# Kernel optimization log

Hardware: AMD Instinct MI355X
Metric: run time of the kernel (lower is better)

## Reference

```python
import jax, jax.numpy as jnp
import numpy as np
from jax import lax

# LIF parameters (norse defaults)
DT = 0.001
TAU_SYN_INV = 200.0
TAU_MEM_INV = 100.0
V_TH = 1.0
V_LEAK = 0.0
V_RESET = 0.0


def _spike(v_minus_th):
    # forward heaviside (surrogate grad only matters for bwd module)
    return (v_minus_th > 0).astype(v_minus_th.dtype)


def setup_inputs() -> dict:
    key = jax.random.key(0)
    ks = jax.random.split(key, 5)
    B, T, F, H, O = 256, 1000, 128, 256, 2
    x = jax.random.normal(ks[0], (B, T, F), dtype=jnp.float32)
    w_in = jax.random.normal(ks[1], (H, F), dtype=jnp.float32) / np.sqrt(F)
    w_rec = jax.random.normal(ks[2], (H, H), dtype=jnp.float32) / np.sqrt(H)
    fc_w = jax.random.normal(ks[3], (O, H), dtype=jnp.float32) / np.sqrt(H)
    fc_b = jnp.zeros((O,), dtype=jnp.float32)
    return {"x": x, "w_in": w_in, "w_rec": w_rec, "fc_w": fc_w, "fc_b": fc_b}


def reference(x, w_in, w_rec, fc_w, fc_b):
    B = x.shape[0]
    H = w_in.shape[0]
    # precompute feed-forward input currents for all timesteps: [B,T,H] -> [T,B,H]
    xw = jnp.einsum("btf,hf->bth", x, w_in)
    xw = jnp.swapaxes(xw, 0, 1)

    def step(carry, xt):
        v, i, z = carry
        # membrane decay toward leak + synaptic current integration
        v_dec = v + DT * TAU_MEM_INV * ((V_LEAK - v) + i)
        # synaptic current decay
        i_dec = i * (1.0 - DT * TAU_SYN_INV)
        # threshold / spike / reset
        z_new = _spike(v_dec - V_TH)
        v_new = (1.0 - z_new) * v_dec + z_new * V_RESET
        # inject feed-forward + recurrent current for next step
        i_new = i_dec + xt + z @ w_rec.T
        return (v_new, i_new, z_new), z_new

    zeros = jnp.zeros((B, H), dtype=x.dtype)
    _, zs = lax.scan(step, (zeros, zeros, zeros), xw)  # zs: [T,B,H]
    total_activity = zs.sum(axis=0)  # sum over time (torch dim=1 batch-first)
    return total_activity @ fc_w.T + fc_b
```

## Files before the change

### kernel.cpp

```cpp
#include <hip/hip_runtime.h>
#include <hip/hip_bf16.h>
#include <stdint.h>

constexpr int B = 256, T = 1000, F = 128, H = 256, O = 2;
constexpr float DT_TAU_MEM = 0.1f;
constexpr float SYN_DECAY  = 0.8f;
constexpr float V_THRESH   = 1.0f;

__device__ inline unsigned short f2bf_raw(float f) {
  __hip_bfloat16 b = __float2bfloat16(f);
  return *reinterpret_cast<unsigned short*>(&b);
}

template <typename XT> struct XConv;
template <> struct XConv<float> {
  static __device__ inline float load(const float* p) { return *p; }
  static __device__ inline void store4(float* p, float a, float b, float c, float d) {
    *reinterpret_cast<float4*>(p) = make_float4(a, b, c, d);
  }
};
template <> struct XConv<__hip_bfloat16> {
  static __device__ inline float load(const __hip_bfloat16* p) { return __bfloat162float(*p); }
  static __device__ inline void store4(__hip_bfloat16* p, float a, float b, float c, float d) {
    ushort4 u = make_ushort4(f2bf_raw(a), f2bf_raw(b), f2bf_raw(c), f2bf_raw(d));
    *reinterpret_cast<ushort4*>(p) = u;
  }
};

__global__ void transpose_wrec(const float* __restrict__ w, float* __restrict__ wT) {
  int k = blockIdx.x;
  int h = threadIdx.x;
  wT[k * H + h] = w[h * H + k];
}

template <typename XT>
__global__ __launch_bounds__(256) void gemm_xw(const float* __restrict__ x,
                                               const float* __restrict__ w_in,
                                               XT* __restrict__ xw) {
  constexpr int K = 128;
  constexpr int SA = 68;
  __shared__ float As[K][SA];
  __shared__ float Bs[K][SA];

  const int m0 = blockIdx.x * 64;
  const int n0 = blockIdx.y * 64;
  const int tid = threadIdx.x;

  {
    const int r  = tid >> 2;
    const int cq = tid & 3;
    const float* xa = x    + (size_t)(m0 + r) * K;
    const float* xb = w_in + (size_t)(n0 + r) * K;
#pragma unroll
    for (int j = 0; j < 8; ++j) {
      const int c = (cq + (j << 2)) << 2;
      float4 av = *reinterpret_cast<const float4*>(xa + c);
      float4 bv = *reinterpret_cast<const float4*>(xb + c);
      As[c + 0][r] = av.x; As[c + 1][r] = av.y; As[c + 2][r] = av.z; As[c + 3][r] = av.w;
      Bs[c + 0][r] = bv.x; Bs[c + 1][r] = bv.y; Bs[c + 2][r] = bv.z; Bs[c + 3][r] = bv.w;
    }
  }
  __syncthreads();

  const int tn = (tid & 15) << 2;
  const int tm = (tid >> 4) << 2;
  float acc[4][4] = {};

#pragma unroll 16
  for (int k = 0; k < K; ++k) {
    float4 a = *reinterpret_cast<const float4*>(&As[k][tm]);
    float4 b = *reinterpret_cast<const float4*>(&Bs[k][tn]);
    acc[0][0] += a.x * b.x; acc[0][1] += a.x * b.y; acc[0][2] += a.x * b.z; acc[0][3] += a.x * b.w;
    acc[1][0] += a.y * b.x; acc[1][1] += a.y * b.y; acc[1][2] += a.y * b.z; acc[1][3] += a.y * b.w;
    acc[2][0] += a.z * b.x; acc[2][1] += a.z * b.y; acc[2][2] += a.z * b.z; acc[2][3] += a.z * b.w;
    acc[3][0] += a.w * b.x; acc[3][1] += a.w * b.y; acc[3][2] += a.w * b.z; acc[3][3] += a.w * b.w;
  }

#pragma unroll
  for (int im = 0; im < 4; ++im) {
    XT* p = xw + (size_t)(m0 + tm + im) * H + (n0 + tn);
    XConv<XT>::store4(p, acc[im][0], acc[im][1], acc[im][2], acc[im][3]);
  }
}

template <typename XT>
__global__ __launch_bounds__(256) void scan_lif(const XT* __restrict__ xw,
                                                const float* __restrict__ wT,
                                                const float* __restrict__ fc_w,
                                                const float* __restrict__ fc_b,
                                                float* __restrict__ out) {
  const int b = blockIdx.x;
  const int h = threadIdx.x;

  __shared__ int   spk[2][H];
  __shared__ int   cnt[2];
  __shared__ float red[8];

  if (h < 2) cnt[h] = 0;
  __syncthreads();

  float v = 0.f, cur = 0.f;
  int spike_count = 0;

  const XT* xrow = xw + (size_t)b * T * H + h;
  float x0 = XConv<XT>::load(xrow);
  float x1 = XConv<XT>::load(xrow + H);

  for (int t = 0; t < T; ++t) {
    const int cb = t & 1, nb = cb ^ 1;
    const float xt = x0;
    x0 = x1;
    x1 = (t + 2 < T) ? XConv<XT>::load(xrow + (size_t)(t + 2) * H) : 0.f;

    float rec = 0.f;
    const int c = cnt[cb];
    int j = 0;
    for (; j + 4 <= c; j += 4) {
      const int k0 = spk[cb][j + 0], k1 = spk[cb][j + 1];
      const int k2 = spk[cb][j + 2], k3 = spk[cb][j + 3];
      const float w0 = wT[(k0 << 8) + h];
      const float w1 = wT[(k1 << 8) + h];
      const float w2 = wT[(k2 << 8) + h];
      const float w3 = wT[(k3 << 8) + h];
      rec += (w0 + w1) + (w2 + w3);
    }
    for (; j < c; ++j) rec += wT[(spk[cb][j] << 8) + h];

    const float v_dec = v + DT_TAU_MEM * (cur - v);
    const int z = v_dec > V_THRESH;
    v = z ? 0.f : v_dec;
    cur = cur * SYN_DECAY + xt + rec;
    spike_count += z;

    __syncthreads();
    if (z) { int p = atomicAdd(&cnt[nb], 1); spk[nb][p] = h; }
    if (h == 0) cnt[cb] = 0;
    __syncthreads();
  }

  const float cf = (float)spike_count;
#pragma unroll
  for (int o = 0; o < O; ++o) {
    float p = cf * fc_w[o * H + h];
#pragma unroll
    for (int off = 32; off > 0; off >>= 1) p += __shfl_down(p, off, 64);
    if ((h & 63) == 0) red[o * 4 + (h >> 6)] = p;
    __syncthreads();
  }
  if (h < O) {
    out[b * O + h] = (red[h * 4 + 0] + red[h * 4 + 1] + red[h * 4 + 2] + red[h * 4 + 3]) + fc_b[h];
  }
}

extern "C" void kernel_launch(void* const* d_in, const int* in_sizes, int n_in,
                              void* d_out, int out_size, void* d_ws, size_t ws_size,
                              hipStream_t stream) {
  const float* x     = (const float*)d_in[0];
  const float* w_in  = (const float*)d_in[1];
  const float* w_rec = (const float*)d_in[2];
  const float* fc_w  = (const float*)d_in[3];
  const float* fc_b  = (const float*)d_in[4];
  float* out = (float*)d_out;

  float* wT = (float*)d_ws;
  const size_t wT_bytes = (size_t)H * H * sizeof(float);
  char* xw_base = (char*)d_ws + wT_bytes;
  const size_t xw_elems = (size_t)B * T * H;
  const bool use_f32 = ws_size >= wT_bytes + xw_elems * sizeof(float);

  transpose_wrec<<<H, H, 0, stream>>>(w_rec, wT);

  if (use_f32) {
    float* xw = (float*)xw_base;
    gemm_xw<float><<<dim3(B * T / 64, H / 64), 256, 0, stream>>>(x, w_in, xw);
    scan_lif<float><<<B, H, 0, stream>>>(xw, wT, fc_w, fc_b, out);
  } else {
    __hip_bfloat16* xw = (__hip_bfloat16*)xw_base;
    gemm_xw<__hip_bfloat16><<<dim3(B * T / 64, H / 64), 256, 0, stream>>>(x, w_in, xw);
    scan_lif<__hip_bfloat16><<<B, H, 0, stream>>>(xw, wT, fc_w, fc_b, out);
  }
}
```

Measured before the change: 1.172 ms.

## Run LIF scan as single wavefront with ballot spike masks and LDS-cached weights

The scan kernel now runs one 64-lane wavefront per batch row, each lane owning four neurons. Spike lists come from wavefront ballots instead of shared-memory atomics, which removes both per-step __syncthreads barriers. Half of the transposed recurrent weights (128 rows as float4) are cached in LDS and the rest read from global, gathered in predicated chunks of eight to keep loads in flight. The cost is far fewer threads per block and heavy register use, which limits latency hiding, and the global half of the weights still pays memory latency.

```diff
diff --git a/kernel.cpp b/kernel.cpp
--- a/kernel.cpp
+++ b/kernel.cpp
@@ -14,13 +14,21 @@
 
 template <typename XT> struct XConv;
 template <> struct XConv<float> {
-  static __device__ inline float load(const float* p) { return *p; }
+  static __device__ inline float4 load4(const float* p) {
+    return *reinterpret_cast<const float4*>(p);
+  }
   static __device__ inline void store4(float* p, float a, float b, float c, float d) {
     *reinterpret_cast<float4*>(p) = make_float4(a, b, c, d);
   }
 };
 template <> struct XConv<__hip_bfloat16> {
-  static __device__ inline float load(const __hip_bfloat16* p) { return __bfloat162float(*p); }
+  static __device__ inline float4 load4(const __hip_bfloat16* p) {
+    ushort4 u = *reinterpret_cast<const ushort4*>(p);
+    return make_float4(__uint_as_float((unsigned)u.x << 16),
+                       __uint_as_float((unsigned)u.y << 16),
+                       __uint_as_float((unsigned)u.z << 16),
+                       __uint_as_float((unsigned)u.w << 16));
+  }
   static __device__ inline void store4(__hip_bfloat16* p, float a, float b, float c, float d) {
     ushort4 u = make_ushort4(f2bf_raw(a), f2bf_raw(b), f2bf_raw(c), f2bf_raw(d));
     *reinterpret_cast<ushort4*>(p) = u;
@@ -83,72 +91,148 @@
   }
 }
 
+
+#define EX1(X, Y, ROW) do {                                         \
+    uint64_t sel_ = (X) ? (X) : (Y);                                \
+    int p_ = __builtin_ctzll(sel_ | 0x8000000000000000ull);         \
+    ROW = ((p_ & 31) << 2) | (p_ >> 5) | ((X) ? 0 : 2);             \
+    uint64_t cl_ = sel_ & (sel_ - 1ull);                            \
+    Y = (X) ? (Y) : cl_;                                            \
+    X = (X) ? cl_ : (X);                                            \
+  } while (0)
+
+#define CHUNK8(X, Y, N, BASE, V0,V1,V2,V3,V4,V5,V6,V7, P0,P1,P2,P3,P4,P5,P6,P7) do { \
+    int r_;                                                          \
+    P0 = ((N) > 0) ? 1.f : 0.f; EX1(X, Y, r_); V0 = (BASE)[r_ << 6]; \
+    P1 = ((N) > 1) ? 1.f : 0.f; EX1(X, Y, r_); V1 = (BASE)[r_ << 6]; \
+    P2 = ((N) > 2) ? 1.f : 0.f; EX1(X, Y, r_); V2 = (BASE)[r_ << 6]; \
+    P3 = ((N) > 3) ? 1.f : 0.f; EX1(X, Y, r_); V3 = (BASE)[r_ << 6]; \
+    P4 = ((N) > 4) ? 1.f : 0.f; EX1(X, Y, r_); V4 = (BASE)[r_ << 6]; \
+    P5 = ((N) > 5) ? 1.f : 0.f; EX1(X, Y, r_); V5 = (BASE)[r_ << 6]; \
+    P6 = ((N) > 6) ? 1.f : 0.f; EX1(X, Y, r_); V6 = (BASE)[r_ << 6]; \
+    P7 = ((N) > 7) ? 1.f : 0.f; EX1(X, Y, r_); V7 = (BASE)[r_ << 6]; \
+  } while (0)
+
+#define ACC8(V0,V1,V2,V3,V4,V5,V6,V7, P0,P1,P2,P3,P4,P5,P6,P7) do {  \
+    r0 += P0 * V0.x; r1 += P0 * V0.y; r2 += P0 * V0.z; r3 += P0 * V0.w; \
+    r0 += P1 * V1.x; r1 += P1 * V1.y; r2 += P1 * V1.z; r3 += P1 * V1.w; \
+    r0 += P2 * V2.x; r1 += P2 * V2.y; r2 += P2 * V2.z; r3 += P2 * V2.w; \
+    r0 += P3 * V3.x; r1 += P3 * V3.y; r2 += P3 * V3.z; r3 += P3 * V3.w; \
+    r0 += P4 * V4.x; r1 += P4 * V4.y; r2 += P4 * V4.z; r3 += P4 * V4.w; \
+    r0 += P5 * V5.x; r1 += P5 * V5.y; r2 += P5 * V5.z; r3 += P5 * V5.w; \
+    r0 += P6 * V6.x; r1 += P6 * V6.y; r2 += P6 * V6.z; r3 += P6 * V6.w; \
+    r0 += P7 * V7.x; r1 += P7 * V7.y; r2 += P7 * V7.z; r3 += P7 * V7.w; \
+  } while (0)
+
 template <typename XT>
-__global__ __launch_bounds__(256) void scan_lif(const XT* __restrict__ xw,
-                                                const float* __restrict__ wT,
-                                                const float* __restrict__ fc_w,
-                                                const float* __restrict__ fc_b,
-                                                float* __restrict__ out) {
-  const int b = blockIdx.x;
-  const int h = threadIdx.x;
-
-  __shared__ int   spk[2][H];
-  __shared__ int   cnt[2];
-  __shared__ float red[8];
-
-  if (h < 2) cnt[h] = 0;
+__global__ __launch_bounds__(64, 1) void scan_lif(const XT* __restrict__ xw,
+                                                  const float* __restrict__ wT,
+                                                  const float* __restrict__ fc_w,
+                                                  const float* __restrict__ fc_b,
+                                                  float* __restrict__ out) {
+  const int b  = blockIdx.x;
+  const int ln = threadIdx.x;
+
+  __shared__ float4 wlds[128 * 64];
+
+  const float4* wTf4 = reinterpret_cast<const float4*>(wT);
+  for (int i = ln; i < 128 * 64; i += 64) wlds[i] = wTf4[i];
   __syncthreads();
 
-  float v = 0.f, cur = 0.f;
-  int spike_count = 0;
-
-  const XT* xrow = xw + (size_t)b * T * H + h;
-  float x0 = XConv<XT>::load(xrow);
-  float x1 = XConv<XT>::load(xrow + H);
-
-  for (int t = 0; t < T; ++t) {
-    const int cb = t & 1, nb = cb ^ 1;
-    const float xt = x0;
-    x0 = x1;
-    x1 = (t + 2 < T) ? XConv<XT>::load(xrow + (size_t)(t + 2) * H) : 0.f;
-
-    float rec = 0.f;
-    const int c = cnt[cb];
-    int j = 0;
-    for (; j + 4 <= c; j += 4) {
-      const int k0 = spk[cb][j + 0], k1 = spk[cb][j + 1];
-      const int k2 = spk[cb][j + 2], k3 = spk[cb][j + 3];
-      const float w0 = wT[(k0 << 8) + h];
-      const float w1 = wT[(k1 << 8) + h];
-      const float w2 = wT[(k2 << 8) + h];
-      const float w3 = wT[(k3 << 8) + h];
-      rec += (w0 + w1) + (w2 + w3);
-    }
-    for (; j < c; ++j) rec += wT[(spk[cb][j] << 8) + h];
-
-    const float v_dec = v + DT_TAU_MEM * (cur - v);
-    const int z = v_dec > V_THRESH;
-    v = z ? 0.f : v_dec;
-    cur = cur * SYN_DECAY + xt + rec;
-    spike_count += z;
-
-    __syncthreads();
-    if (z) { int p = atomicAdd(&cnt[nb], 1); spk[nb][p] = h; }
-    if (h == 0) cnt[cb] = 0;
-    __syncthreads();
-  }
-
-  const float cf = (float)spike_count;
+  const float4* gB = wTf4 + 128 * 64 + ln;
+  const float4* lB = &wlds[ln];
+
+  float v0 = 0.f, v1 = 0.f, v2 = 0.f, v3 = 0.f;
+  float c0 = 0.f, c1 = 0.f, c2 = 0.f, c3 = 0.f;
+  int   n0 = 0,   n1 = 0,   n2 = 0,   n3 = 0;
+  unsigned long long mA = 0, mBm = 0, mC = 0, mD = 0;
+
+  const XT* xrow = xw + (size_t)b * T * H + (ln << 2);
+  float4 xa = XConv<XT>::load4(xrow);
+  float4 xb = XConv<XT>::load4(xrow + H);
+
+#pragma unroll 1
+  for (int tt = 0; tt < T; ++tt) {
+    const float4 xt = xa;
+    xa = xb;
+    xb = (tt + 2 < T) ? XConv<XT>::load4(xrow + (size_t)(tt + 2) * H)
+                      : make_float4(0.f, 0.f, 0.f, 0.f);
+
+    uint64_t Lx = (uint32_t)mA         | ((uint64_t)(uint32_t)mBm         << 32);
+    uint64_t Ly = (uint32_t)mC         | ((uint64_t)(uint32_t)mD          << 32);
+    uint64_t Gx = (uint32_t)(mA >> 32) | ((uint64_t)(uint32_t)(mBm >> 32) << 32);
+    uint64_t Gy = (uint32_t)(mC >> 32) | ((uint64_t)(uint32_t)(mD  >> 32) << 32);
+    int nl = __popcll(Lx) + __popcll(Ly);
+    int ng = __popcll(Gx) + __popcll(Gy);
+
+    float r0 = 0.f, r1 = 0.f, r2 = 0.f, r3 = 0.f;
+
+    float4 g0, g1, g2, g3, g4, g5, g6, g7;
+    float  q0, q1, q2, q3, q4, q5, q6, q7;
+    float4 h0, h1, h2, h3, h4, h5, h6, h7;
+    float  u0, u1, u2, u3, u4, u5, u6, u7;
+
+    const bool anyG = (ng > 0);
+    if (anyG) {
+      CHUNK8(Gx, Gy, ng, gB, g0,g1,g2,g3,g4,g5,g6,g7, q0,q1,q2,q3,q4,q5,q6,q7);
+      ng -= 8;
+    }
+
+    while (nl > 0) {
+      float4 l0, l1, l2, l3, l4, l5, l6, l7;
+      float  s0, s1, s2, s3, s4, s5, s6, s7;
+      CHUNK8(Lx, Ly, nl, lB, l0,l1,l2,l3,l4,l5,l6,l7, s0,s1,s2,s3,s4,s5,s6,s7);
+      nl -= 8;
+      ACC8(l0,l1,l2,l3,l4,l5,l6,l7, s0,s1,s2,s3,s4,s5,s6,s7);
+    }
+
+    if (anyG) {
+      for (;;) {
+        if (ng <= 0) { ACC8(g0,g1,g2,g3,g4,g5,g6,g7, q0,q1,q2,q3,q4,q5,q6,q7); break; }
+        CHUNK8(Gx, Gy, ng, gB, h0,h1,h2,h3,h4,h5,h6,h7, u0,u1,u2,u3,u4,u5,u6,u7);
+        ng -= 8;
+        ACC8(g0,g1,g2,g3,g4,g5,g6,g7, q0,q1,q2,q3,q4,q5,q6,q7);
+        if (ng <= 0) { ACC8(h0,h1,h2,h3,h4,h5,h6,h7, u0,u1,u2,u3,u4,u5,u6,u7); break; }
+        CHUNK8(Gx, Gy, ng, gB, g0,g1,g2,g3,g4,g5,g6,g7, q0,q1,q2,q3,q4,q5,q6,q7);
+        ng -= 8;
+        ACC8(h0,h1,h2,h3,h4,h5,h6,h7, u0,u1,u2,u3,u4,u5,u6,u7);
+      }
+    }
+
+    const float vd0 = v0 + DT_TAU_MEM * (c0 - v0);
+    const float vd1 = v1 + DT_TAU_MEM * (c1 - v1);
+    const float vd2 = v2 + DT_TAU_MEM * (c2 - v2);
+    const float vd3 = v3 + DT_TAU_MEM * (c3 - v3);
+    const int z0 = vd0 > V_THRESH;
+    const int z1 = vd1 > V_THRESH;
+    const int z2 = vd2 > V_THRESH;
+    const int z3 = vd3 > V_THRESH;
+    v0 = z0 ? 0.f : vd0;  v1 = z1 ? 0.f : vd1;
+    v2 = z2 ? 0.f : vd2;  v3 = z3 ? 0.f : vd3;
+    c0 = c0 * SYN_DECAY + xt.x + r0;
+    c1 = c1 * SYN_DECAY + xt.y + r1;
+    c2 = c2 * SYN_DECAY + xt.z + r2;
+    c3 = c3 * SYN_DECAY + xt.w + r3;
+    n0 += z0; n1 += z1; n2 += z2; n3 += z3;
+
+    mA  = __ballot(z0);
+    mBm = __ballot(z1);
+    mC  = __ballot(z2);
+    mD  = __ballot(z3);
+  }
+
+  const float4 f0 = *reinterpret_cast<const float4*>(fc_w + 0 * H + (ln << 2));
+  const float4 f1 = *reinterpret_cast<const float4*>(fc_w + 1 * H + (ln << 2));
+  float p0 = (float)n0 * f0.x + (float)n1 * f0.y + (float)n2 * f0.z + (float)n3 * f0.w;
+  float p1 = (float)n0 * f1.x + (float)n1 * f1.y + (float)n2 * f1.z + (float)n3 * f1.w;
 #pragma unroll
-  for (int o = 0; o < O; ++o) {
-    float p = cf * fc_w[o * H + h];
-#pragma unroll
-    for (int off = 32; off > 0; off >>= 1) p += __shfl_down(p, off, 64);
-    if ((h & 63) == 0) red[o * 4 + (h >> 6)] = p;
-    __syncthreads();
-  }
-  if (h < O) {
-    out[b * O + h] = (red[h * 4 + 0] + red[h * 4 + 1] + red[h * 4 + 2] + red[h * 4 + 3]) + fc_b[h];
+  for (int off = 32; off > 0; off >>= 1) {
+    p0 += __shfl_down(p0, off, 64);
+    p1 += __shfl_down(p1, off, 64);
+  }
+  if (ln == 0) {
+    out[b * O + 0] = p0 + fc_b[0];
+    out[b * O + 1] = p1 + fc_b[1];
   }
 }
 
@@ -173,10 +257,10 @@
   if (use_f32) {
     float* xw = (float*)xw_base;
     gemm_xw<float><<<dim3(B * T / 64, H / 64), 256, 0, stream>>>(x, w_in, xw);
-    scan_lif<float><<<B, H, 0, stream>>>(xw, wT, fc_w, fc_b, out);
+    scan_lif<float><<<B, 64, 0, stream>>>(xw, wT, fc_w, fc_b, out);
   } else {
     __hip_bfloat16* xw = (__hip_bfloat16*)xw_base;
     gemm_xw<__hip_bfloat16><<<dim3(B * T / 64, H / 64), 256, 0, stream>>>(x, w_in, xw);
-    scan_lif<__hip_bfloat16><<<B, H, 0, stream>>>(xw, wT, fc_w, fc_b, out);
-  }
-}
+    scan_lif<__hip_bfloat16><<<B, 64, 0, stream>>>(xw, wT, fc_w, fc_b, out);
+  }
+}
```

Result: slower. 1.396 ms (+19.2%).

## Rewrite LIF scan with ballot spike bitmasks, LDS-cached weights and batched prefetch

Applied to the files above, without the earlier changes.

Replaces the atomic spike-list construction with per-wave ballot bitmasks in shared memory, so each step needs one barrier instead of two. Spiking rows are extracted with ctz on wave-uniform masks. The first half of the transposed recurrent weights is cached in 128KB of LDS, and the gathers are software-pipelined in chunks of eight with predicated accumulation. Input currents are prefetched eight steps ahead. The cost is one block per CU because of the large LDS use, plus much larger unrolled code and more register pressure.

```diff
diff --git a/kernel.cpp b/kernel.cpp
--- a/kernel.cpp
+++ b/kernel.cpp
@@ -14,13 +14,16 @@
 
 template <typename XT> struct XConv;
 template <> struct XConv<float> {
-  static __device__ inline float load(const float* p) { return *p; }
+  static __device__ inline float load1(const float* p) { return *p; }
   static __device__ inline void store4(float* p, float a, float b, float c, float d) {
     *reinterpret_cast<float4*>(p) = make_float4(a, b, c, d);
   }
 };
 template <> struct XConv<__hip_bfloat16> {
-  static __device__ inline float load(const __hip_bfloat16* p) { return __bfloat162float(*p); }
+  static __device__ inline float load1(const __hip_bfloat16* p) {
+    unsigned u = *reinterpret_cast<const unsigned short*>(p);
+    return __uint_as_float(u << 16);
+  }
   static __device__ inline void store4(__hip_bfloat16* p, float a, float b, float c, float d) {
     ushort4 u = make_ushort4(f2bf_raw(a), f2bf_raw(b), f2bf_raw(c), f2bf_raw(d));
     *reinterpret_cast<ushort4*>(p) = u;
@@ -83,72 +86,184 @@
   }
 }
 
+
+__device__ __forceinline__ uint64_t rl64(uint64_t v) {
+  unsigned lo = __builtin_amdgcn_readfirstlane((unsigned)(v & 0xffffffffull));
+  unsigned hi = __builtin_amdgcn_readfirstlane((unsigned)(v >> 32));
+  return ((uint64_t)hi << 32) | lo;
+}
+
+#define EXS(X, Y, ROW) do {                                          \
+    uint64_t sel_ = (X) ? (X) : (Y);                                 \
+    int p_ = __builtin_ctzll(sel_ | 0x8000000000000000ull);          \
+    ROW = p_ + ((X) ? 0 : 64);                                       \
+    uint64_t cl_ = sel_ & (sel_ - 1ull);                             \
+    Y = (X) ? (Y) : cl_;                                             \
+    X = (X) ? cl_ : (X);                                             \
+  } while (0)
+
+#define CH8(X, Y, N, BASE, V0,V1,V2,V3,V4,V5,V6,V7, P0,P1,P2,P3,P4,P5,P6,P7) do { \
+    int r_;                                                           \
+    P0 = ((N) > 0) ? 1.f : 0.f; EXS(X, Y, r_); V0 = (BASE)[r_ << 8]; \
+    P1 = ((N) > 1) ? 1.f : 0.f; EXS(X, Y, r_); V1 = (BASE)[r_ << 8]; \
+    P2 = ((N) > 2) ? 1.f : 0.f; EXS(X, Y, r_); V2 = (BASE)[r_ << 8]; \
+    P3 = ((N) > 3) ? 1.f : 0.f; EXS(X, Y, r_); V3 = (BASE)[r_ << 8]; \
+    P4 = ((N) > 4) ? 1.f : 0.f; EXS(X, Y, r_); V4 = (BASE)[r_ << 8]; \
+    P5 = ((N) > 5) ? 1.f : 0.f; EXS(X, Y, r_); V5 = (BASE)[r_ << 8]; \
+    P6 = ((N) > 6) ? 1.f : 0.f; EXS(X, Y, r_); V6 = (BASE)[r_ << 8]; \
+    P7 = ((N) > 7) ? 1.f : 0.f; EXS(X, Y, r_); V7 = (BASE)[r_ << 8]; \
+  } while (0)
+
+#define AC8(V0,V1,V2,V3,V4,V5,V6,V7, P0,P1,P2,P3,P4,P5,P6,P7) do {   \
+    r0 += P0 * V0; r1 += P1 * V1; r2 += P2 * V2; r3 += P3 * V3;      \
+    r0 += P4 * V4; r1 += P5 * V5; r2 += P6 * V6; r3 += P7 * V7;      \
+  } while (0)
+
+#define STEP(J, XTV) do {                                                     \
+    uint64_t M0 = rl64(msk[((J)&1)^1][0]);                                    \
+    uint64_t M1 = rl64(msk[((J)&1)^1][1]);                                    \
+    uint64_t M2 = rl64(msk[((J)&1)^1][2]);                                    \
+    uint64_t M3 = rl64(msk[((J)&1)^1][3]);                                    \
+    int nl = __popcll(M0) + __popcll(M1);                                     \
+    int ng = __popcll(M2) + __popcll(M3);                                     \
+    float r0 = 0.f, r1 = 0.f, r2 = 0.f, r3 = 0.f;                             \
+    float ga0,ga1,ga2,ga3,ga4,ga5,ga6,ga7;                                    \
+    float qa0,qa1,qa2,qa3,qa4,qa5,qa6,qa7;                                    \
+    float gb0,gb1,gb2,gb3,gb4,gb5,gb6,gb7;                                    \
+    float qb0,qb1,qb2,qb3,qb4,qb5,qb6,qb7;                                    \
+    const bool anyG = (ng > 0);                                               \
+    if (anyG) {                                                               \
+      CH8(M2,M3,ng,gBase, ga0,ga1,ga2,ga3,ga4,ga5,ga6,ga7,                    \
+          qa0,qa1,qa2,qa3,qa4,qa5,qa6,qa7);                                   \
+      ng -= 8;                                                                \
+    }                                                                         \
+    if (nl > 0) {                                                             \
+      float la0,la1,la2,la3,la4,la5,la6,la7;                                  \
+      float sa0,sa1,sa2,sa3,sa4,sa5,sa6,sa7;                                  \
+      float lb0,lb1,lb2,lb3,lb4,lb5,lb6,lb7;                                  \
+      float sb0,sb1,sb2,sb3,sb4,sb5,sb6,sb7;                                  \
+      CH8(M0,M1,nl,lBase, la0,la1,la2,la3,la4,la5,la6,la7,                    \
+          sa0,sa1,sa2,sa3,sa4,sa5,sa6,sa7);                                   \
+      nl -= 8;                                                                \
+      for (;;) {                                                              \
+        if (nl <= 0) { AC8(la0,la1,la2,la3,la4,la5,la6,la7,                   \
+                           sa0,sa1,sa2,sa3,sa4,sa5,sa6,sa7); break; }         \
+        CH8(M0,M1,nl,lBase, lb0,lb1,lb2,lb3,lb4,lb5,lb6,lb7,                  \
+            sb0,sb1,sb2,sb3,sb4,sb5,sb6,sb7);                                 \
+        nl -= 8;                                                              \
+        AC8(la0,la1,la2,la3,la4,la5,la6,la7,                                  \
+            sa0,sa1,sa2,sa3,sa4,sa5,sa6,sa7);                                 \
+        if (nl <= 0) { AC8(lb0,lb1,lb2,lb3,lb4,lb5,lb6,lb7,                   \
+                           sb0,sb1,sb2,sb3,sb4,sb5,sb6,sb7); break; }         \
+        CH8(M0,M1,nl,lBase, la0,la1,la2,la3,la4,la5,la6,la7,                  \
+            sa0,sa1,sa2,sa3,sa4,sa5,sa6,sa7);                                 \
+        nl -= 8;                                                              \
+        AC8(lb0,lb1,lb2,lb3,lb4,lb5,lb6,lb7,                                  \
+            sb0,sb1,sb2,sb3,sb4,sb5,sb6,sb7);                                 \
+      }                                                                       \
+    }                                                                         \
+    if (anyG) {                                                               \
+      for (;;) {                                                              \
+        if (ng <= 0) { AC8(ga0,ga1,ga2,ga3,ga4,ga5,ga6,ga7,                   \
+                           qa0,qa1,qa2,qa3,qa4,qa5,qa6,qa7); break; }         \
+        CH8(M2,M3,ng,gBase, gb0,gb1,gb2,gb3,gb4,gb5,gb6,gb7,                  \
+            qb0,qb1,qb2,qb3,qb4,qb5,qb6,qb7);                                 \
+        ng -= 8;                                                              \
+        AC8(ga0,ga1,ga2,ga3,ga4,ga5,ga6,ga7,                                  \
+            qa0,qa1,qa2,qa3,qa4,qa5,qa6,qa7);                                 \
+        if (ng <= 0) { AC8(gb0,gb1,gb2,gb3,gb4,gb5,gb6,gb7,                   \
+                           qb0,qb1,qb2,qb3,qb4,qb5,qb6,qb7); break; }         \
+        CH8(M2,M3,ng,gBase, ga0,ga1,ga2,ga3,ga4,ga5,ga6,ga7,                  \
+            qa0,qa1,qa2,qa3,qa4,qa5,qa6,qa7);                                 \
+        ng -= 8;                                                              \
+        AC8(gb0,gb1,gb2,gb3,gb4,gb5,gb6,gb7,                                  \
+            qb0,qb1,qb2,qb3,qb4,qb5,qb6,qb7);                                 \
+      }                                                                       \
+    }                                                                         \
+    const float rec = (r0 + r1) + (r2 + r3);                                  \
+    const float vd = v + DT_TAU_MEM * (cur - v);                              \
+    const int z = vd > V_THRESH;                                              \
+    v = z ? 0.f : vd;                                                         \
+    cur = cur * SYN_DECAY + (XTV) + rec;                                      \
+    ncnt += z;                                                                \
+    unsigned long long bz = __ballot(z);                                      \
+    if (ln == 0) msk[(J)&1][w] = bz;                                          \
+    __syncthreads();                                                          \
+  } while (0)
+
 template <typename XT>
-__global__ __launch_bounds__(256) void scan_lif(const XT* __restrict__ xw,
-                                                const float* __restrict__ wT,
-                                                const float* __restrict__ fc_w,
-                                                const float* __restrict__ fc_b,
-                                                float* __restrict__ out) {
-  const int b = blockIdx.x;
-  const int h = threadIdx.x;
-
-  __shared__ int   spk[2][H];
-  __shared__ int   cnt[2];
+__global__ __launch_bounds__(256, 1) void scan_lif(const XT* __restrict__ xw,
+                                                   const float* __restrict__ wT,
+                                                   const float* __restrict__ fc_w,
+                                                   const float* __restrict__ fc_b,
+                                                   float* __restrict__ out) {
+  const int b   = blockIdx.x;
+  const int tid = threadIdx.x;
+  const int w   = tid >> 6;
+  const int ln  = tid & 63;
+
+  __shared__ float wlds[128 * 256];
+  __shared__ unsigned long long msk[2][4];
   __shared__ float red[8];
 
-  if (h < 2) cnt[h] = 0;
+  {
+    const float4* srcv = reinterpret_cast<const float4*>(wT);
+    float4* dstv = reinterpret_cast<float4*>(wlds);
+    for (int i = tid; i < 8192; i += 256) dstv[i] = srcv[i];
+  }
+  if (tid < 4) msk[1][tid] = 0ull;
+
+  const float* lBase = wlds + tid;
+  const float* gBase = wT + 32768 + tid;
+
+  float v = 0.f, cur = 0.f;
+  int ncnt = 0;
+
+  const XT* xrow = xw + (size_t)b * T * H + tid;
+  float xc0 = XConv<XT>::load1(xrow + 0 * H);
+  float xc1 = XConv<XT>::load1(xrow + 1 * H);
+  float xc2 = XConv<XT>::load1(xrow + 2 * H);
+  float xc3 = XConv<XT>::load1(xrow + 3 * H);
+  float xc4 = XConv<XT>::load1(xrow + 4 * H);
+  float xc5 = XConv<XT>::load1(xrow + 5 * H);
+  float xc6 = XConv<XT>::load1(xrow + 6 * H);
+  float xc7 = XConv<XT>::load1(xrow + 7 * H);
+  float xn0, xn1, xn2, xn3, xn4, xn5, xn6, xn7;
+
   __syncthreads();
 
-  float v = 0.f, cur = 0.f;
-  int spike_count = 0;
-
-  const XT* xrow = xw + (size_t)b * T * H + h;
-  float x0 = XConv<XT>::load(xrow);
-  float x1 = XConv<XT>::load(xrow + H);
-
-  for (int t = 0; t < T; ++t) {
-    const int cb = t & 1, nb = cb ^ 1;
-    const float xt = x0;
-    x0 = x1;
-    x1 = (t + 2 < T) ? XConv<XT>::load(xrow + (size_t)(t + 2) * H) : 0.f;
-
-    float rec = 0.f;
-    const int c = cnt[cb];
-    int j = 0;
-    for (; j + 4 <= c; j += 4) {
-      const int k0 = spk[cb][j + 0], k1 = spk[cb][j + 1];
-      const int k2 = spk[cb][j + 2], k3 = spk[cb][j + 3];
-      const float w0 = wT[(k0 << 8) + h];
-      const float w1 = wT[(k1 << 8) + h];
-      const float w2 = wT[(k2 << 8) + h];
-      const float w3 = wT[(k3 << 8) + h];
-      rec += (w0 + w1) + (w2 + w3);
+  for (int blk = 0; blk < 125; ++blk) {
+    if (blk < 124) {
+      const XT* nx = xrow + (size_t)(blk + 1) * 8 * H;
+      xn0 = XConv<XT>::load1(nx + 0 * H);
+      xn1 = XConv<XT>::load1(nx + 1 * H);
+      xn2 = XConv<XT>::load1(nx + 2 * H);
+      xn3 = XConv<XT>::load1(nx + 3 * H);
+      xn4 = XConv<XT>::load1(nx + 4 * H);
+      xn5 = XConv<XT>::load1(nx + 5 * H);
+      xn6 = XConv<XT>::load1(nx + 6 * H);
+      xn7 = XConv<XT>::load1(nx + 7 * H);
+    } else {
+      xn0 = xn1 = xn2 = xn3 = xn4 = xn5 = xn6 = xn7 = 0.f;
     }
-    for (; j < c; ++j) rec += wT[(spk[cb][j] << 8) + h];
-
-    const float v_dec = v + DT_TAU_MEM * (cur - v);
-    const int z = v_dec > V_THRESH;
-    v = z ? 0.f : v_dec;
-    cur = cur * SYN_DECAY + xt + rec;
-    spike_count += z;
-
+    STEP(0, xc0); STEP(1, xc1); STEP(2, xc2); STEP(3, xc3);
+    STEP(4, xc4); STEP(5, xc5); STEP(6, xc6); STEP(7, xc7);
+    xc0 = xn0; xc1 = xn1; xc2 = xn2; xc3 = xn3;
+    xc4 = xn4; xc5 = xn5; xc6 = xn6; xc7 = xn7;
+  }
+
+  const float cf = (float)ncnt;
+#pragma unroll
+  for (int o = 0; o < O; ++o) {
+    float p = cf * fc_w[o * H + tid];
+#pragma unroll
+    for (int off = 32; off > 0; off >>= 1) p += __shfl_down(p, off, 64);
+    if (ln == 0) red[o * 4 + w] = p;
     __syncthreads();
-    if (z) { int p = atomicAdd(&cnt[nb], 1); spk[nb][p] = h; }
-    if (h == 0) cnt[cb] = 0;
-    __syncthreads();
-  }
-
-  const float cf = (float)spike_count;
-#pragma unroll
-  for (int o = 0; o < O; ++o) {
-    float p = cf * fc_w[o * H + h];
-#pragma unroll
-    for (int off = 32; off > 0; off >>= 1) p += __shfl_down(p, off, 64);
-    if ((h & 63) == 0) red[o * 4 + (h >> 6)] = p;
-    __syncthreads();
-  }
-  if (h < O) {
-    out[b * O + h] = (red[h * 4 + 0] + red[h * 4 + 1] + red[h * 4 + 2] + red[h * 4 + 3]) + fc_b[h];
+  }
+  if (tid < O) {
+    out[b * O + tid] =
+        (red[tid * 4 + 0] + red[tid * 4 + 1] + red[tid * 4 + 2] + red[tid * 4 + 3]) + fc_b[tid];
   }
 }
 
@@ -173,10 +288,10 @@
   if (use_f32) {
     float* xw = (float*)xw_base;
     gemm_xw<float><<<dim3(B * T / 64, H / 64), 256, 0, stream>>>(x, w_in, xw);
-    scan_lif<float><<<B, H, 0, stream>>>(xw, wT, fc_w, fc_b, out);
+    scan_lif<float><<<B, 256, 0, stream>>>(xw, wT, fc_w, fc_b, out);
   } else {
     __hip_bfloat16* xw = (__hip_bfloat16*)xw_base;
     gemm_xw<__hip_bfloat16><<<dim3(B * T / 64, H / 64), 256, 0, stream>>>(x, w_in, xw);
-    scan_lif<__hip_bfloat16><<<B, H, 0, stream>>>(xw, wT, fc_w, fc_b, out);
-  }
-}
+    scan_lif<__hip_bfloat16><<<B, 256, 0, stream>>>(xw, wT, fc_w, fc_b, out);
+  }
+}
```

New measurement: 1.406 ms. 1.2x slower.

## Replace atomic spike list with ballot masks and software-pipelined recurrent gathers

Applied to the files above, without the earlier changes.

The spike list built with shared atomics is replaced by per-wave ballot masks broadcast through LDS, so each step needs one barrier instead of two. Recurrent weight rows are gathered with a fixed 16-per-wave issue pattern into double-buffered registers, so loads for the next step overlap the accumulate of the current one. Overflow beyond 16 spikes per wave falls back to a serial path. Half of the transposed w_rec, padded with a zero row, is staged in LDS and the other half read from global memory, and xw inputs are prefetched in chunks of eight steps. This costs many registers and one block per CU, and the zero-row trick pays for 64 loads per step even when few neurons spike.

```diff
diff --git a/kernel.cpp b/kernel.cpp
--- a/kernel.cpp
+++ b/kernel.cpp
@@ -7,6 +7,9 @@
 constexpr float SYN_DECAY  = 0.8f;
 constexpr float V_THRESH   = 1.0f;
 
+constexpr int NRB = 65;
+constexpr int WREGION_FLOATS = 4 * NRB * H;
+
 __device__ inline unsigned short f2bf_raw(float f) {
   __hip_bfloat16 b = __float2bfloat16(f);
   return *reinterpret_cast<unsigned short*>(&b);
@@ -14,23 +17,32 @@
 
 template <typename XT> struct XConv;
 template <> struct XConv<float> {
-  static __device__ inline float load(const float* p) { return *p; }
+  static __device__ inline float load1(const float* p) { return *p; }
   static __device__ inline void store4(float* p, float a, float b, float c, float d) {
     *reinterpret_cast<float4*>(p) = make_float4(a, b, c, d);
   }
 };
 template <> struct XConv<__hip_bfloat16> {
-  static __device__ inline float load(const __hip_bfloat16* p) { return __bfloat162float(*p); }
+  static __device__ inline float load1(const __hip_bfloat16* p) {
+    unsigned u = *reinterpret_cast<const unsigned short*>(p);
+    return __uint_as_float(u << 16);
+  }
   static __device__ inline void store4(__hip_bfloat16* p, float a, float b, float c, float d) {
     ushort4 u = make_ushort4(f2bf_raw(a), f2bf_raw(b), f2bf_raw(c), f2bf_raw(d));
     *reinterpret_cast<ushort4*>(p) = u;
   }
 };
 
-__global__ void transpose_wrec(const float* __restrict__ w, float* __restrict__ wT) {
-  int k = blockIdx.x;
+__global__ void transpose_wrec(const float* __restrict__ w, float* __restrict__ wz) {
+  int j = blockIdx.x;
   int h = threadIdx.x;
-  wT[k * H + h] = w[h * H + k];
+  int s = j / NRB, u = j % NRB;
+  float val = 0.f;
+  if (u != 0) {
+    int k = s * 64 + (u - 1);
+    val = w[h * H + k];
+  }
+  wz[(size_t)j * H + h] = val;
 }
 
 template <typename XT>
@@ -83,72 +95,138 @@
   }
 }
 
+
+__device__ __forceinline__ uint64_t rl64(uint64_t v) {
+  unsigned lo = __builtin_amdgcn_readfirstlane((unsigned)(v & 0xffffffffull));
+  unsigned hi = __builtin_amdgcn_readfirstlane((unsigned)(v >> 32));
+  return ((uint64_t)hi << 32) | lo;
+}
+
+#define ISSUE16(M, PTR, BUF, OFS) do {                                  \
+    _Pragma("unroll")                                                   \
+    for (int _i = 0; _i < 16; ++_i) {                                   \
+      int p_ = (M) ? (int)__builtin_ctzll(M) : -1;                      \
+      unsigned u_ = (((unsigned)p_) << 10) + 1024u;                     \
+      (BUF)[(OFS) + _i] = *(const float*)((const char*)(PTR) + u_);     \
+      (M) &= (M) - 1ull;                                                \
+    }                                                                   \
+  } while (0)
+
+#define ACC16(BUF, OFS) do {                                            \
+    _Pragma("unroll")                                                   \
+    for (int _i = 0; _i < 16; ++_i) racc[_i & 3] += (BUF)[(OFS) + _i];  \
+  } while (0)
+
+#define SLOWADD(M, PTR) while (M) {                                     \
+    int p_ = (int)__builtin_ctzll(M);                                   \
+    unsigned u_ = (((unsigned)p_) << 10) + 1024u;                       \
+    racc[0] += *(const float*)((const char*)(PTR) + u_);                \
+    (M) &= (M) - 1ull;                                                  \
+  }
+
+#define STEP(IB, CB, RI0, RI1, RI2, RI3, RC0, RC1, RC2, RC3, PAR, XWV) do { \
+          \
+    uint64_t _m0 = M0, _m1 = M1, _m2 = M2, _m3 = M3;                        \
+    ISSUE16(_m0, lptr0, IB, 0);                                             \
+    ISSUE16(_m1, lptr1, IB, 16);                                            \
+    ISSUE16(_m2, gptr2, IB, 32);                                            \
+    ISSUE16(_m3, gptr3, IB, 48);                                            \
+    RI0 = _m0; RI1 = _m1; RI2 = _m2; RI3 = _m3;                             \
+       \
+    float racc[4] = {0.f, 0.f, 0.f, 0.f};                                   \
+    ACC16(CB, 32); ACC16(CB, 48);                                           \
+    ACC16(CB, 0);  ACC16(CB, 16);                                           \
+    if (__builtin_expect((RC0 | RC1 | RC2 | RC3) != 0ull, 0)) {             \
+      SLOWADD(RC0, lptr0); SLOWADD(RC1, lptr1);                             \
+      SLOWADD(RC2, gptr2); SLOWADD(RC3, gptr3);                             \
+      __builtin_amdgcn_s_waitcnt(0);          \
+    }                                                                       \
+    const float rec = (racc[0] + racc[1]) + (racc[2] + racc[3]);            \
+                                             \
+    cur = cur * SYN_DECAY + (XWV) + rec;                                    \
+                                        \
+    const float vd = v + DT_TAU_MEM * (cur - v);                            \
+    const int z = vd > V_THRESH;                                            \
+    v = z ? 0.f : vd;                                                       \
+    ncnt += z;                                                              \
+                                 \
+    unsigned long long bz = __ballot(z);                                    \
+    if (ln == 0) mskbuf[PAR][w] = bz;                                       \
+    __syncthreads();                                                        \
+    M0 = rl64(mskbuf[PAR][0]); M1 = rl64(mskbuf[PAR][1]);                   \
+    M2 = rl64(mskbuf[PAR][2]); M3 = rl64(mskbuf[PAR][3]);                   \
+  } while (0)
+
 template <typename XT>
-__global__ __launch_bounds__(256) void scan_lif(const XT* __restrict__ xw,
-                                                const float* __restrict__ wT,
-                                                const float* __restrict__ fc_w,
-                                                const float* __restrict__ fc_b,
-                                                float* __restrict__ out) {
-  const int b = blockIdx.x;
-  const int h = threadIdx.x;
-
-  __shared__ int   spk[2][H];
-  __shared__ int   cnt[2];
+__global__ __launch_bounds__(256, 1) void scan_lif(const XT* __restrict__ xw,
+                                                   const float* __restrict__ wz,
+                                                   const float* __restrict__ fc_w,
+                                                   const float* __restrict__ fc_b,
+                                                   float* __restrict__ out) {
+  const int b   = blockIdx.x;
+  const int tid = threadIdx.x;
+  const int w   = tid >> 6;
+  const int ln  = tid & 63;
+
+  __shared__ float wlds[2 * NRB][H];
+  __shared__ unsigned long long mskbuf[2][4];
   __shared__ float red[8];
 
-  if (h < 2) cnt[h] = 0;
+  {
+    const float4* s4 = reinterpret_cast<const float4*>(wz);
+    float4* d4 = reinterpret_cast<float4*>(&wlds[0][0]);
+    for (int i = tid; i < 2 * NRB * H / 4; i += 256) d4[i] = s4[i];
+  }
+
+  const char* lptr0 = (const char*)&wlds[0][0]        + tid * 4;
+  const char* lptr1 = (const char*)&wlds[NRB][0]      + tid * 4;
+  const char* gptr2 = (const char*)(wz + 2 * NRB * H) + tid * 4;
+  const char* gptr3 = (const char*)(wz + 3 * NRB * H) + tid * 4;
+
+  float v = 0.f, cur = 0.f;
+  int ncnt = 0;
+  uint64_t M0 = 0, M1 = 0, M2 = 0, M3 = 0;
+  uint64_t RA0 = 0, RA1 = 0, RA2 = 0, RA3 = 0;
+  uint64_t RB0 = 0, RB1 = 0, RB2 = 0, RB3 = 0;
+
+  float bufA[64], bufB[64];
+#pragma unroll
+  for (int i = 0; i < 64; ++i) { bufA[i] = 0.f; bufB[i] = 0.f; }
+
+  const XT* xrow = xw + (size_t)b * T * H + tid;
+  float xprev = 0.f;
+  float xc[8];
+
   __syncthreads();
 
-  float v = 0.f, cur = 0.f;
-  int spike_count = 0;
-
-  const XT* xrow = xw + (size_t)b * T * H + h;
-  float x0 = XConv<XT>::load(xrow);
-  float x1 = XConv<XT>::load(xrow + H);
-
-  for (int t = 0; t < T; ++t) {
-    const int cb = t & 1, nb = cb ^ 1;
-    const float xt = x0;
-    x0 = x1;
-    x1 = (t + 2 < T) ? XConv<XT>::load(xrow + (size_t)(t + 2) * H) : 0.f;
-
-    float rec = 0.f;
-    const int c = cnt[cb];
-    int j = 0;
-    for (; j + 4 <= c; j += 4) {
-      const int k0 = spk[cb][j + 0], k1 = spk[cb][j + 1];
-      const int k2 = spk[cb][j + 2], k3 = spk[cb][j + 3];
-      const float w0 = wT[(k0 << 8) + h];
-      const float w1 = wT[(k1 << 8) + h];
-      const float w2 = wT[(k2 << 8) + h];
-      const float w3 = wT[(k3 << 8) + h];
-      rec += (w0 + w1) + (w2 + w3);
-    }
-    for (; j < c; ++j) rec += wT[(spk[cb][j] << 8) + h];
-
-    const float v_dec = v + DT_TAU_MEM * (cur - v);
-    const int z = v_dec > V_THRESH;
-    v = z ? 0.f : v_dec;
-    cur = cur * SYN_DECAY + xt + rec;
-    spike_count += z;
-
+  for (int blk = 0; blk < 125; ++blk) {
+    const XT* nx = xrow + (size_t)blk * 8 * H;
+#pragma unroll
+    for (int j = 0; j < 8; ++j) xc[j] = XConv<XT>::load1(nx + j * H);
+
+    STEP(bufA, bufB, RA0, RA1, RA2, RA3, RB0, RB1, RB2, RB3, 0, xprev);
+    STEP(bufB, bufA, RB0, RB1, RB2, RB3, RA0, RA1, RA2, RA3, 1, xc[0]);
+    STEP(bufA, bufB, RA0, RA1, RA2, RA3, RB0, RB1, RB2, RB3, 0, xc[1]);
+    STEP(bufB, bufA, RB0, RB1, RB2, RB3, RA0, RA1, RA2, RA3, 1, xc[2]);
+    STEP(bufA, bufB, RA0, RA1, RA2, RA3, RB0, RB1, RB2, RB3, 0, xc[3]);
+    STEP(bufB, bufA, RB0, RB1, RB2, RB3, RA0, RA1, RA2, RA3, 1, xc[4]);
+    STEP(bufA, bufB, RA0, RA1, RA2, RA3, RB0, RB1, RB2, RB3, 0, xc[5]);
+    STEP(bufB, bufA, RB0, RB1, RB2, RB3, RA0, RA1, RA2, RA3, 1, xc[6]);
+    xprev = xc[7];
+  }
+
+  const float cf = (float)ncnt;
+#pragma unroll
+  for (int o = 0; o < O; ++o) {
+    float p = cf * fc_w[o * H + tid];
+#pragma unroll
+    for (int off = 32; off > 0; off >>= 1) p += __shfl_down(p, off, 64);
+    if (ln == 0) red[o * 4 + w] = p;
     __syncthreads();
-    if (z) { int p = atomicAdd(&cnt[nb], 1); spk[nb][p] = h; }
-    if (h == 0) cnt[cb] = 0;
-    __syncthreads();
-  }
-
-  const float cf = (float)spike_count;
-#pragma unroll
-  for (int o = 0; o < O; ++o) {
-    float p = cf * fc_w[o * H + h];
-#pragma unroll
-    for (int off = 32; off > 0; off >>= 1) p += __shfl_down(p, off, 64);
-    if ((h & 63) == 0) red[o * 4 + (h >> 6)] = p;
-    __syncthreads();
-  }
-  if (h < O) {
-    out[b * O + h] = (red[h * 4 + 0] + red[h * 4 + 1] + red[h * 4 + 2] + red[h * 4 + 3]) + fc_b[h];
+  }
+  if (tid < O) {
+    out[b * O + tid] =
+        (red[tid * 4 + 0] + red[tid * 4 + 1] + red[tid * 4 + 2] + red[tid * 4 + 3]) + fc_b[tid];
   }
 }
 
@@ -162,21 +240,21 @@
   const float* fc_b  = (const float*)d_in[4];
   float* out = (float*)d_out;
 
-  float* wT = (float*)d_ws;
-  const size_t wT_bytes = (size_t)H * H * sizeof(float);
-  char* xw_base = (char*)d_ws + wT_bytes;
+  float* wz = (float*)d_ws;
+  const size_t wz_bytes = (size_t)WREGION_FLOATS * sizeof(float);
+  char* xw_base = (char*)d_ws + wz_bytes;
   const size_t xw_elems = (size_t)B * T * H;
-  const bool use_f32 = ws_size >= wT_bytes + xw_elems * sizeof(float);
-
-  transpose_wrec<<<H, H, 0, stream>>>(w_rec, wT);
+  const bool use_f32 = ws_size >= wz_bytes + xw_elems * sizeof(float);
+
+  transpose_wrec<<<4 * NRB, H, 0, stream>>>(w_rec, wz);
 
   if (use_f32) {
     float* xw = (float*)xw_base;
     gemm_xw<float><<<dim3(B * T / 64, H / 64), 256, 0, stream>>>(x, w_in, xw);
-    scan_lif<float><<<B, H, 0, stream>>>(xw, wT, fc_w, fc_b, out);
+    scan_lif<float><<<B, 256, 0, stream>>>(xw, wz, fc_w, fc_b, out);
   } else {
     __hip_bfloat16* xw = (__hip_bfloat16*)xw_base;
     gemm_xw<__hip_bfloat16><<<dim3(B * T / 64, H / 64), 256, 0, stream>>>(x, w_in, xw);
-    scan_lif<__hip_bfloat16><<<B, H, 0, stream>>>(xw, wT, fc_w, fc_b, out);
-  }
-}
+    scan_lif<__hip_bfloat16><<<B, 256, 0, stream>>>(xw, wz, fc_w, fc_b, out);
+  }
+}
```

Result: slower. 1.912 ms (+63.2%).
